# Performance work log

Measured on AMD Instinct MI355X. Metric: run time of the kernel, lower is better.

## Reference

```python
import jax, jax.numpy as jnp
import numpy as np

N = 20000        # genes
E = 100000       # edges per relation
D_IN = 512
HID = 64         # hidden_dim (per-head channels in layers 0,1)
HEADS = 8
D_H = HID * HEADS   # 512 hidden width
D_OUT = 256
NEG_SLOPE = 0.2  # GATv2Conv default negative_slope


def _gatv2(x, src, dst, Wl, bl, Wr, br, att, out_bias, heads, ch):
    """PyG GATv2Conv, add_self_loops=False, concat=True, eval mode (no dropout)."""
    n = x.shape[0]
    xl = (x @ Wl + bl).reshape(n, heads, ch)   # lin_l (source transform)
    xr = (x @ Wr + br).reshape(n, heads, ch)   # lin_r (target transform)
    e = jax.nn.leaky_relu(xl[src] + xr[dst], NEG_SLOPE)   # [E,H,C]
    score = jnp.einsum('ehc,hc->eh', e, att)              # [E,H]
    # segment softmax over incoming edges of each destination node
    m = jax.ops.segment_max(score, dst, num_segments=n)   # [N,H]
    w = jnp.exp(score - m[dst])
    z = jax.ops.segment_sum(w, dst, num_segments=n)
    alpha = w / z[dst]
    out = jax.ops.segment_sum(alpha[:, :, None] * xl[src], dst, num_segments=n)
    return out.reshape(n, heads * ch) + out_bias


def _layernorm(x, g, b):
    mu = x.mean(-1, keepdims=True)
    var = x.var(-1, keepdims=True)
    return (x - mu) * jax.lax.rsqrt(var + 1e-5) * g + b


def setup_inputs() -> dict:
    key = jax.random.key(0)
    ks = jax.random.split(key, 12)
    gn = lambda k, shape, fan_in: (jax.random.normal(k, shape, dtype=jnp.float32)
                                   / np.float32(np.sqrt(fan_in)))
    inp = {}
    inp['x'] = jax.random.normal(ks[0], (N, D_IN), dtype=jnp.float32)
    inp['edge_index'] = jax.random.randint(ks[1], (3, 2, E), 0, N, dtype=jnp.int32)
    # input projection  Linear(512 -> 512)
    inp['proj_w'] = gn(ks[2], (D_IN, D_H), D_IN)
    inp['proj_b'] = jnp.zeros((D_H,), jnp.float32)
    # layers 0,1: stacked over [layer, edge_type]
    inp['l01_lin_l_w'] = gn(ks[3], (2, 3, D_H, D_H), D_H)
    inp['l01_lin_l_b'] = jnp.zeros((2, 3, D_H), jnp.float32)
    inp['l01_lin_r_w'] = gn(ks[4], (2, 3, D_H, D_H), D_H)
    inp['l01_lin_r_b'] = jnp.zeros((2, 3, D_H), jnp.float32)
    inp['l01_att'] = gn(ks[5], (2, 3, HEADS, HID), HID)
    inp['l01_bias'] = jnp.zeros((2, 3, D_H), jnp.float32)
    # layer 2: heads=1, out_channels=256, stacked over edge_type
    inp['l2_lin_l_w'] = gn(ks[6], (3, D_H, D_OUT), D_H)
    inp['l2_lin_l_b'] = jnp.zeros((3, D_OUT), jnp.float32)
    inp['l2_lin_r_w'] = gn(ks[7], (3, D_H, D_OUT), D_H)
    inp['l2_lin_r_b'] = jnp.zeros((3, D_OUT), jnp.float32)
    inp['l2_att'] = gn(ks[8], (3, 1, D_OUT), D_OUT)
    inp['l2_bias'] = jnp.zeros((3, D_OUT), jnp.float32)
    # LayerNorms
    inp['ln01_gamma'] = jnp.ones((2, D_H), jnp.float32)
    inp['ln01_beta'] = jnp.zeros((2, D_H), jnp.float32)
    inp['ln2_gamma'] = jnp.ones((D_OUT,), jnp.float32)
    inp['ln2_beta'] = jnp.zeros((D_OUT,), jnp.float32)
    return inp


def reference(x, edge_index, proj_w, proj_b,
              l01_lin_l_w, l01_lin_l_b, l01_lin_r_w, l01_lin_r_b, l01_att, l01_bias,
              l2_lin_l_w, l2_lin_l_b, l2_lin_r_w, l2_lin_r_b, l2_att, l2_bias,
              ln01_gamma, ln01_beta, ln2_gamma, ln2_beta):
    # input proj + ELU (dropout = identity in eval)
    h = jax.nn.elu(x @ proj_w + proj_b)
    # layers 0 and 1: HeteroConv(sum over 3 relations), ELU, residual, LayerNorm
    for li in range(2):
        res = h
        out = 0.0
        for et in range(3):
            src, dst = edge_index[et, 0], edge_index[et, 1]
            out = out + _gatv2(h, src, dst,
                               l01_lin_l_w[li, et], l01_lin_l_b[li, et],
                               l01_lin_r_w[li, et], l01_lin_r_b[li, et],
                               l01_att[li, et], l01_bias[li, et], HEADS, HID)
        h = jax.nn.elu(out) + res
        h = _layernorm(h, ln01_gamma[li], ln01_beta[li])
    # layer 2: heads=1, out=256; no residual (dims differ)
    out = 0.0
    for et in range(3):
        src, dst = edge_index[et, 0], edge_index[et, 1]
        out = out + _gatv2(h, src, dst,
                           l2_lin_l_w[et], l2_lin_l_b[et],
                           l2_lin_r_w[et], l2_lin_r_b[et],
                           l2_att[et], l2_bias[et], 1, D_OUT)
    h = jax.nn.elu(out)
    return _layernorm(h, ln2_gamma, ln2_beta)
```

## Files before the change

kernel.cpp:

```cpp
#include <hip/hip_runtime.h>


#define NN 20000
#define NE 100000
#define DH 512
#define DOUT 256

typedef __attribute__((ext_vector_type(8))) short short8;
typedef __attribute__((ext_vector_type(4))) short short4v;
typedef __attribute__((ext_vector_type(4))) float f32x4;

__device__ __forceinline__ float b2f(unsigned short s) {
    union { unsigned u; float f; } v; v.u = ((unsigned)s) << 16; return v.f;
}
__device__ __forceinline__ unsigned short f2b(float f) {
    unsigned u = __float_as_uint(f);
    u += 0x7FFFu + ((u >> 16) & 1u);
    return (unsigned short)(u >> 16);
}
__device__ __forceinline__ void load_lds16(const unsigned short* g, unsigned short* l) {
    __builtin_amdgcn_global_load_lds(
        (const __attribute__((address_space(1))) unsigned int*)g,
        (__attribute__((address_space(3))) unsigned int*)l, 16, 0, 0);
}

__global__ void cvt_f2b_k(const float* __restrict__ in,
                          unsigned short* __restrict__ out, int n) {
    int i0 = (blockIdx.x * blockDim.x + threadIdx.x) * 8;
    if (i0 >= n) return;
    #pragma unroll
    for (int j = 0; j < 8; j++) out[i0 + j] = f2b(in[i0 + j]);
}

struct TSeg { const float* in; unsigned short* out; int C; };
struct TTable { TSeg s[19]; };

__global__ void transpose_all_k(TTable t) {
    __shared__ float tile[32][33];
    TSeg d = t.s[blockIdx.y];
    int tiles_x = d.C >> 5;
    int nt = tiles_x << 4;
    if ((int)blockIdx.x >= nt) return;
    int bx = blockIdx.x % tiles_x, by = blockIdx.x / tiles_x;
    int c0 = bx * 32, r0 = by * 32;
    int tx = threadIdx.x & 31, ty = threadIdx.x >> 5;
    #pragma unroll
    for (int i = ty; i < 32; i += 8)
        tile[i][tx] = d.in[(size_t)(r0 + i) * d.C + c0 + tx];
    __syncthreads();
    #pragma unroll
    for (int i = ty; i < 32; i += 8)
        d.out[(size_t)(c0 + i) * 512 + r0 + tx] = f2b(tile[tx][i]);
}

__global__ void count_all_k(const int* __restrict__ ei, int* __restrict__ counts) {
    int i = blockIdx.x * blockDim.x + threadIdx.x;
    if (i >= 3 * NE) return;
    int et = i / NE, idx = i - et * NE;
    int d = ei[(size_t)et * 2 * NE + NE + idx];
    atomicAdd(&counts[et * (NN + 1) + d], 1);
}

__global__ __launch_bounds__(1024)
void scan_par_k(const int* __restrict__ counts, int* __restrict__ offs, int n) {
    __shared__ int part[1024];
    const int* c = counts + (size_t)blockIdx.x * (n + 1);
    int* o = offs + (size_t)blockIdx.x * (n + 1);
    int tid = threadIdx.x;
    int per = (n + 1023) / 1024;
    int base = tid * per;
    int lim = min(base + per, n);
    int sum = 0;
    for (int i = base; i < lim; i++) sum += c[i];
    part[tid] = sum;
    __syncthreads();
    #pragma unroll
    for (int off = 1; off < 1024; off <<= 1) {
        int v = (tid >= off) ? part[tid - off] : 0;
        __syncthreads();
        part[tid] += v;
        __syncthreads();
    }
    int run = part[tid] - sum;
    for (int i = base; i < lim; i++) { o[i] = run; run += c[i]; }
    if (tid == 1023) o[n] = part[1023];
}

__global__ void scatter_all_k(const int* __restrict__ ei, int* __restrict__ cursor,
                              int* __restrict__ srcs_sorted) {
    int i = blockIdx.x * blockDim.x + threadIdx.x;
    if (i >= 3 * NE) return;
    int et = i / NE, idx = i - et * NE;
    int s = ei[(size_t)et * 2 * NE + idx];
    int d = ei[(size_t)et * 2 * NE + NE + idx];
    int p = atomicAdd(&cursor[et * (NN + 1) + d], 1);
    srcs_sorted[(size_t)et * NE + p] = s;
}

template<int ACT, int SEGL2>
__global__ __launch_bounds__(256)
void gemm_k(const unsigned short* __restrict__ A,
            const unsigned short* __restrict__ Bt,
            const float* __restrict__ lb,
            const float* __restrict__ rb,
            unsigned short* __restrict__ Cb,
            int M, int N, int K, int MT, int NT, int STRIPE) {
    __shared__ __align__(16) unsigned short smem[17408];
    unsigned short* As = smem;
    unsigned short* Bs = smem + 8192;
    int bid = blockIdx.x;
    int xcd = bid & 7, r = bid >> 3;
    int mtile = xcd * STRIPE + r / NT;
    int ntile = r % NT;
    if (mtile >= MT) return;
    int bm0 = mtile * 128, bn0 = ntile * 128;

    int tid = threadIdx.x;
    int lane = tid & 63, wave = tid >> 6;
    int quad = lane >> 4, l16 = lane & 15;
    int rw = (wave >> 1) * 64, cw = (wave & 1) * 64;
    int rxor = l16 & 7;

    f32x4 acc[4][4];
    #pragma unroll
    for (int mi = 0; mi < 4; mi++)
        #pragma unroll
        for (int ni = 0; ni < 4; ni++) acc[mi][ni] = (f32x4){0.f, 0.f, 0.f, 0.f};

    for (int k0 = 0; k0 < K; k0 += 64) {
        #pragma unroll
        for (int i = 0; i < 4; i++) {
            int f = i * 256 + tid;
            int row = f >> 3, s = f & 7;
            int cg = s ^ (row & 7);
            load_lds16(A + (size_t)(bm0 + row) * K + k0 + cg * 8, As + f * 8);
        }
        #pragma unroll
        for (int i = 0; i < 4; i++) {
            int f = i * 256 + tid;
            int col = f >> 3, s = f & 7;
            int cg = s ^ (col & 7);
            load_lds16(Bt + (size_t)(bn0 + col) * K + k0 + cg * 8, Bs + f * 8);
        }
        __syncthreads();
        #pragma unroll
        for (int ki = 0; ki < 64; ki += 32) {
            int kch = quad + (ki >> 3);
            int slot = kch ^ rxor;
            short8 af[4], bf[4];
            #pragma unroll
            for (int mi = 0; mi < 4; mi++)
                af[mi] = *(const short8*)(As + (rw + mi * 16 + l16) * 64 + slot * 8);
            #pragma unroll
            for (int ni = 0; ni < 4; ni++)
                bf[ni] = *(const short8*)(Bs + (cw + ni * 16 + l16) * 64 + slot * 8);
            #pragma unroll
            for (int mi = 0; mi < 4; mi++)
                #pragma unroll
                for (int ni = 0; ni < 4; ni++)
                    acc[mi][ni] = __builtin_amdgcn_mfma_f32_16x16x32_bf16(
                        af[mi], bf[ni], acc[mi][ni], 0, 0, 0);
        }
        __syncthreads();
    }

    #pragma unroll
    for (int ni = 0; ni < 4; ni++) {
        int col = cw + ni * 16 + l16;
        int seg = col >> (SEGL2 + 1);
        int lr = (col >> SEGL2) & 1;
        int cc2 = col & ((1 << SEGL2) - 1);
        float bv = (lr ? rb : lb)[(seg << SEGL2) + cc2];
        #pragma unroll
        for (int mi = 0; mi < 4; mi++) {
            int row = rw + mi * 16 + quad * 4;
            #pragma unroll
            for (int i = 0; i < 4; i++) {
                float v = acc[mi][ni][i] + bv;
                if (ACT == 1) v = v > 0.f ? v : expm1f(v);
                smem[(row + i) * 136 + col] = f2b(v);
            }
        }
    }
    __syncthreads();
    #pragma unroll
    for (int it = 0; it < 8; it++) {
        int chunk = it * 256 + tid;
        int row = chunk >> 4, cc = chunk & 15;
        int grow = bm0 + row;
        if (grow < M) {
            uint4 d = *(const uint4*)(smem + row * 136 + cc * 8);
            *(uint4*)(Cb + (size_t)grow * N + bn0 + cc * 8) = d;
        }
    }
}

__global__ __launch_bounds__(192)
void gat_fused01_k(const unsigned short* __restrict__ C,
                   const int* __restrict__ offs3,
                   const int* __restrict__ srcs3,
                   const float* __restrict__ att,
                   const float* __restrict__ bias3,
                   unsigned short* __restrict__ hb,
                   const float* __restrict__ gamma,
                   const float* __restrict__ beta,
                   int n_nodes) {
    const unsigned LD = 3072;
    __shared__ float lds_tot[2 * DH];
    int tid = threadIdx.x;
    int lane = tid & 63, et = tid >> 6;
    int n = blockIdx.x;
    int c0 = lane * 8;

    const int* offs = offs3 + et * (NN + 1);
    const int* srcs = srcs3 + (size_t)et * NE;
    int e0 = offs[n], e1 = offs[n + 1];

    float tot[8];
    #pragma unroll
    for (int j = 0; j < 8; j++) tot[j] = 0.f;

    if (e0 < e1) {
        const unsigned short* XL = C + et * 1024 + c0;
        float xr[8], at[8];
        {
            short8 t = *(const short8*)(C + (size_t)n * LD + et * 1024 + 512 + c0);
            #pragma unroll
            for (int j = 0; j < 8; j++) xr[j] = b2f((unsigned short)t[j]);
            #pragma unroll
            for (int j = 0; j < 8; j++) at[j] = att[et * 512 + c0 + j];
        }
        float z = 0.f, acc[8];
        #pragma unroll
        for (int j = 0; j < 8; j++) acc[j] = 0.f;

        auto G = [&](int idx) {
            return *(const short8*)(XL + (unsigned)srcs[idx] * LD);
        };
        auto process = [&](short8 cur) {
            float xl[8];
            #pragma unroll
            for (int j = 0; j < 8; j++) xl[j] = b2f((unsigned short)cur[j]);
            float p = 0.f;
            #pragma unroll
            for (int j = 0; j < 8; j++) {
                float v = xl[j] + xr[j];
                v = fmaxf(v, 0.2f * v);
                p = fmaf(v, at[j], p);
            }
            p += __shfl_xor(p, 1, 64);
            p += __shfl_xor(p, 2, 64);
            p += __shfl_xor(p, 4, 64);
            float wgt = __expf(p);
            z += wgt;
            #pragma unroll
            for (int j = 0; j < 8; j++) acc[j] = fmaf(wgt, xl[j], acc[j]);
        };

        int ef = e0, eb = e1 - 1;
        short8 a0 = G(ef);
        short8 a1 = G(min(ef + 1, eb));
        short8 b0 = G(eb);
        short8 b1 = G(max(eb - 1, ef));
        while (ef < eb) {
            short8 ca = a0; a0 = a1; a1 = G(min(ef + 2, eb));
            short8 cb = b0; b0 = b1; b1 = G(max(eb - 2, ef));
            process(ca);
            process(cb);
            ef++; eb--;
        }
        if (ef == eb) process(a0);

        float inv = 1.f / z;
        #pragma unroll
        for (int j = 0; j < 8; j++) tot[j] = acc[j] * inv;
    }

    if (et) {
        float* dst = lds_tot + (et - 1) * DH + lane;
        #pragma unroll
        for (int j = 0; j < 8; j++) dst[j * 64] = tot[j];
    }
    __syncthreads();
    if (et == 0) {
        unsigned short* hrow = hb + (size_t)n * DH + c0;
        short8 rt = *(const short8*)hrow;
        float v[8]; float s1 = 0.f;
        #pragma unroll
        for (int j = 0; j < 8; j++) {
            int c = c0 + j;
            float x = tot[j] + lds_tot[j * 64 + lane] + lds_tot[DH + j * 64 + lane]
                    + bias3[c] + bias3[512 + c] + bias3[1024 + c];
            x = x > 0.f ? x : expm1f(x);
            x += b2f((unsigned short)rt[j]);
            v[j] = x; s1 += x;
        }
        #pragma unroll
        for (int off = 1; off < 64; off <<= 1) s1 += __shfl_xor(s1, off, 64);
        float mean = s1 * (1.f / DH);
        float s2 = 0.f;
        #pragma unroll
        for (int j = 0; j < 8; j++) { float d = v[j] - mean; s2 += d * d; }
        #pragma unroll
        for (int off = 1; off < 64; off <<= 1) s2 += __shfl_xor(s2, off, 64);
        float rstd = rsqrtf(s2 * (1.f / DH) + 1e-5f);
        short8 ov;
        #pragma unroll
        for (int j = 0; j < 8; j++) {
            int c = c0 + j;
            ov[j] = (short)f2b((v[j] - mean) * rstd * gamma[c] + beta[c]);
        }
        *(short8*)hrow = ov;
    }
    (void)n_nodes;
}

__global__ __launch_bounds__(192)
void gat_fused2_k(const unsigned short* __restrict__ C,
                  const int* __restrict__ offs3,
                  const int* __restrict__ srcs3,
                  const float* __restrict__ att,
                  const float* __restrict__ bias3,
                  const float* __restrict__ gamma,
                  const float* __restrict__ beta,
                  float* __restrict__ out, int n_nodes) {
    const unsigned LD = 1536;
    __shared__ float lds_tot[2 * DOUT];
    int tid = threadIdx.x;
    int lane = tid & 63, et = tid >> 6;
    int n = blockIdx.x;
    int c0 = lane * 4;

    const int* offs = offs3 + et * (NN + 1);
    const int* srcs = srcs3 + (size_t)et * NE;
    int e0 = offs[n], e1 = offs[n + 1];

    float tot[4] = {0.f, 0.f, 0.f, 0.f};

    if (e0 < e1) {
        const unsigned short* XL = C + et * 512 + c0;
        float xr[4], at[4];
        {
            short4v t = *(const short4v*)(C + (size_t)n * LD + et * 512 + 256 + c0);
            #pragma unroll
            for (int j = 0; j < 4; j++) xr[j] = b2f((unsigned short)t[j]);
            #pragma unroll
            for (int j = 0; j < 4; j++) at[j] = att[et * 256 + c0 + j];
        }
        float z = 0.f, acc[4] = {0.f, 0.f, 0.f, 0.f};

        auto G = [&](int idx) {
            return *(const short4v*)(XL + (unsigned)srcs[idx] * LD);
        };
        auto process = [&](short4v cur) {
            float xl[4];
            #pragma unroll
            for (int j = 0; j < 4; j++) xl[j] = b2f((unsigned short)cur[j]);
            float p = 0.f;
            #pragma unroll
            for (int j = 0; j < 4; j++) {
                float v = xl[j] + xr[j];
                v = fmaxf(v, 0.2f * v);
                p = fmaf(v, at[j], p);
            }
            #pragma unroll
            for (int off = 1; off < 64; off <<= 1) p += __shfl_xor(p, off, 64);
            float wgt = __expf(p);
            z += wgt;
            #pragma unroll
            for (int j = 0; j < 4; j++) acc[j] = fmaf(wgt, xl[j], acc[j]);
        };

        int ef = e0, eb = e1 - 1;
        short4v a0 = G(ef);
        short4v a1 = G(min(ef + 1, eb));
        short4v b0 = G(eb);
        short4v b1 = G(max(eb - 1, ef));
        while (ef < eb) {
            short4v ca = a0; a0 = a1; a1 = G(min(ef + 2, eb));
            short4v cb = b0; b0 = b1; b1 = G(max(eb - 2, ef));
            process(ca);
            process(cb);
            ef++; eb--;
        }
        if (ef == eb) process(a0);

        float inv = 1.f / z;
        #pragma unroll
        for (int j = 0; j < 4; j++) tot[j] = acc[j] * inv;
    }

    if (et) {
        float* dst = lds_tot + (et - 1) * DOUT + lane;
        #pragma unroll
        for (int j = 0; j < 4; j++) dst[j * 64] = tot[j];
    }
    __syncthreads();
    if (et == 0) {
        float v[4]; float s1 = 0.f;
        #pragma unroll
        for (int j = 0; j < 4; j++) {
            int c = c0 + j;
            float x = tot[j] + lds_tot[j * 64 + lane] + lds_tot[DOUT + j * 64 + lane]
                    + bias3[c] + bias3[256 + c] + bias3[512 + c];
            x = x > 0.f ? x : expm1f(x);
            v[j] = x; s1 += x;
        }
        #pragma unroll
        for (int off = 1; off < 64; off <<= 1) s1 += __shfl_xor(s1, off, 64);
        float mean = s1 * (1.f / DOUT);
        float s2 = 0.f;
        #pragma unroll
        for (int j = 0; j < 4; j++) { float d = v[j] - mean; s2 += d * d; }
        #pragma unroll
        for (int off = 1; off < 64; off <<= 1) s2 += __shfl_xor(s2, off, 64);
        float rstd = rsqrtf(s2 * (1.f / DOUT) + 1e-5f);
        f32x4 o;
        #pragma unroll
        for (int j = 0; j < 4; j++) {
            int c = c0 + j;
            o[j] = (v[j] - mean) * rstd * gamma[c] + beta[c];
        }
        *(f32x4*)(out + (size_t)n * DOUT + c0) = o;
    }
    (void)n_nodes;
}

extern "C" void kernel_launch(void* const* d_in, const int* in_sizes, int n_in,
                              void* d_out, int out_size, void* d_ws, size_t ws_size,
                              hipStream_t stream) {
    const float* x       = (const float*)d_in[0];
    const int*   ei      = (const int*)d_in[1];
    const float* proj_w  = (const float*)d_in[2];
    const float* proj_b  = (const float*)d_in[3];
    const float* l01lw   = (const float*)d_in[4];
    const float* l01lb   = (const float*)d_in[5];
    const float* l01rw   = (const float*)d_in[6];
    const float* l01rb   = (const float*)d_in[7];
    const float* l01att  = (const float*)d_in[8];
    const float* l01bias = (const float*)d_in[9];
    const float* l2lw    = (const float*)d_in[10];
    const float* l2lb    = (const float*)d_in[11];
    const float* l2rw    = (const float*)d_in[12];
    const float* l2rb    = (const float*)d_in[13];
    const float* l2att   = (const float*)d_in[14];
    const float* l2bias  = (const float*)d_in[15];
    const float* g01     = (const float*)d_in[16];
    const float* b01     = (const float*)d_in[17];
    const float* g2      = (const float*)d_in[18];
    const float* b2      = (const float*)d_in[19];
    (void)in_sizes; (void)n_in; (void)out_size; (void)ws_size;

    char* w = (char*)d_ws;
    size_t off = 0;
    auto carve = [&](size_t bytes) { void* p = w + off; off = (off + bytes + 255) & ~(size_t)255; return p; };
    unsigned short* h_b     = (unsigned short*)carve((size_t)NN * DH * 2);
    unsigned short* xb      = (unsigned short*)carve((size_t)NN * DH * 2);
    unsigned short* Cbuf    = (unsigned short*)carve((size_t)NN * 3072 * 2);
    unsigned short* Wt      = (unsigned short*)carve((size_t)4194304 * 2);
    int*            counts3 = (int*)           carve((size_t)3 * (NN + 1) * 4);
    int*            offs3   = (int*)           carve((size_t)3 * (NN + 1) * 4);
    int*            srcs3   = (int*)           carve((size_t)3 * NE * 4);
    carve(65536);

    unsigned short* Wt_proj = Wt;
    unsigned short* Wt_L0   = Wt_proj + 262144;
    unsigned short* Wt_L1   = Wt_L0 + 3072 * 512;
    unsigned short* Wt_L2   = Wt_L1 + 3072 * 512;

    dim3 tb(256);
    const int MT = (NN + 127) / 128;
    const int STRIPE = (MT + 7) / 8;

    cvt_f2b_k<<<dim3(5000), tb, 0, stream>>>(x, xb, NN * DH);
    TTable tt;
    {
        int s = 0;
        tt.s[s++] = {proj_w, Wt_proj, 512};
        for (int li = 0; li < 2; li++) {
            unsigned short* base = li ? Wt_L1 : Wt_L0;
            for (int et = 0; et < 3; et++)
                tt.s[s++] = {l01lw + (size_t)(li * 3 + et) * 262144,
                             base + (size_t)et * 2 * 262144, 512};
            for (int et = 0; et < 3; et++)
                tt.s[s++] = {l01rw + (size_t)(li * 3 + et) * 262144,
                             base + 262144 + (size_t)et * 2 * 262144, 512};
        }
        for (int et = 0; et < 3; et++)
            tt.s[s++] = {l2lw + (size_t)et * 131072,
                         Wt_L2 + (size_t)et * 2 * 131072, 256};
        for (int et = 0; et < 3; et++)
            tt.s[s++] = {l2rw + (size_t)et * 131072,
                         Wt_L2 + 131072 + (size_t)et * 2 * 131072, 256};
    }
    transpose_all_k<<<dim3(256, 19), tb, 0, stream>>>(tt);

    hipMemsetAsync(counts3, 0, (size_t)3 * (NN + 1) * 4, stream);
    count_all_k<<<dim3((3 * NE + 255) / 256), tb, 0, stream>>>(ei, counts3);
    scan_par_k<<<dim3(3), dim3(1024), 0, stream>>>(counts3, offs3, NN);
    hipMemcpyAsync(counts3, offs3, (size_t)3 * (NN + 1) * 4,
                   hipMemcpyDeviceToDevice, stream);
    scatter_all_k<<<dim3((3 * NE + 255) / 256), tb, 0, stream>>>(ei, counts3, srcs3);

    gemm_k<1, 9><<<dim3(8 * STRIPE * 4), tb, 0, stream>>>(
        xb, Wt_proj, proj_b, proj_b, h_b, NN, 512, 512, MT, 4, STRIPE);

    for (int li = 0; li < 2; li++) {
        gemm_k<0, 9><<<dim3(8 * STRIPE * 24), tb, 0, stream>>>(
            h_b, li ? Wt_L1 : Wt_L0,
            l01lb + (size_t)li * 3 * 512, l01rb + (size_t)li * 3 * 512,
            Cbuf, NN, 3072, 512, MT, 24, STRIPE);
        gat_fused01_k<<<dim3(NN), dim3(192), 0, stream>>>(
            Cbuf, offs3, srcs3,
            l01att + (size_t)li * 3 * 512, l01bias + (size_t)li * 3 * 512,
            h_b, g01 + (size_t)li * DH, b01 + (size_t)li * DH, NN);
    }

    gemm_k<0, 8><<<dim3(8 * STRIPE * 12), tb, 0, stream>>>(
        h_b, Wt_L2, l2lb, l2rb, Cbuf, NN, 1536, 512, MT, 12, STRIPE);
    gat_fused2_k<<<dim3(NN), dim3(192), 0, stream>>>(
        Cbuf, offs3, srcs3, l2att, l2bias, g2, b2, (float*)d_out, NN);
}
```

Measured before the change: 642.5 us.

## Replace 128x128 GEMM with 256x256 double-buffered LDS-prefetch GEMM kernel

Swaps the 128x128, 256-thread bf16 MFMA GEMM for a 256x256, 512-thread kernel. It double-buffers A/B tiles in LDS and issues the next k-tile's global-to-LDS loads between the MFMA phases, raising wave priority around the MFMA blocks. Larger tiles raise operand reuse per LDS load and the prefetch is meant to hide global latency. The cost is a 128KB LDS footprint (one block per CU), more grid quantization/tail effects over 79 row tiles, and a two-pass epilogue to stage the output through LDS.

```diff
diff --git a/kernel.cpp b/kernel.cpp
--- a/kernel.cpp
+++ b/kernel.cpp
@@ -98,99 +98,138 @@
 }
 
 template<int ACT, int SEGL2>
-__global__ __launch_bounds__(256)
-void gemm_k(const unsigned short* __restrict__ A,
-            const unsigned short* __restrict__ Bt,
-            const float* __restrict__ lb,
-            const float* __restrict__ rb,
-            unsigned short* __restrict__ Cb,
-            int M, int N, int K, int MT, int NT, int STRIPE) {
-    __shared__ __align__(16) unsigned short smem[17408];
-    unsigned short* As = smem;
-    unsigned short* Bs = smem + 8192;
+__global__ __launch_bounds__(512, 2)
+void gemm256_k(const unsigned short* __restrict__ A,
+               const unsigned short* __restrict__ Bt,
+               const float* __restrict__ lb,
+               const float* __restrict__ rb,
+               unsigned short* __restrict__ Cb,
+               int M, int N, int K, int MT, int NT) {
+    __shared__ __align__(16) unsigned short smem[65536];
+
     int bid = blockIdx.x;
-    int xcd = bid & 7, r = bid >> 3;
-    int mtile = xcd * STRIPE + r / NT;
-    int ntile = r % NT;
-    if (mtile >= MT) return;
-    int bm0 = mtile * 128, bn0 = ntile * 128;
+    int nwg = MT * NT;
+    int q = nwg >> 3, r = nwg & 7;
+    int xcd = bid & 7;
+    int wg = (xcd < r ? xcd * (q + 1) : r * (q + 1) + (xcd - r) * q) + (bid >> 3);
+    int mtile = wg / NT, ntile = wg % NT;
+    int bm0 = mtile * 256, bn0 = ntile * 256;
 
     int tid = threadIdx.x;
-    int lane = tid & 63, wave = tid >> 6;
+    int lane = tid & 63, wid = tid >> 6;
+    int wr = wid >> 2, wc = wid & 3;
     int quad = lane >> 4, l16 = lane & 15;
-    int rw = (wave >> 1) * 64, cw = (wave & 1) * 64;
+    int rbase = wr * 128, cbase = wc * 64;
     int rxor = l16 & 7;
 
-    f32x4 acc[4][4];
-    #pragma unroll
-    for (int mi = 0; mi < 4; mi++)
-        #pragma unroll
-        for (int ni = 0; ni < 4; ni++) acc[mi][ni] = (f32x4){0.f, 0.f, 0.f, 0.f};
-
-    for (int k0 = 0; k0 < K; k0 += 64) {
-        #pragma unroll
-        for (int i = 0; i < 4; i++) {
-            int f = i * 256 + tid;
-            int row = f >> 3, s = f & 7;
-            int cg = s ^ (row & 7);
-            load_lds16(A + (size_t)(bm0 + row) * K + k0 + cg * 8, As + f * 8);
-        }
-        #pragma unroll
-        for (int i = 0; i < 4; i++) {
-            int f = i * 256 + tid;
-            int col = f >> 3, s = f & 7;
-            int cg = s ^ (col & 7);
-            load_lds16(Bt + (size_t)(bn0 + col) * K + k0 + cg * 8, Bs + f * 8);
-        }
+    f32x4 acc[8][4];
+    #pragma unroll
+    for (int m = 0; m < 8; m++)
+        #pragma unroll
+        for (int n = 0; n < 4; n++) acc[m][n] = (f32x4){0.f, 0.f, 0.f, 0.f};
+
+    const int NKT = K >> 6;
+
+    #pragma unroll
+    for (int ld = 0; ld < 4; ld++) {
+        int f = ld * 512 + tid;
+        int row = f >> 3, s = f & 7;
+        int cg = s ^ (row & 7);
+        load_lds16(A + (size_t)(bm0 + row) * K + cg * 8, smem + f * 8);
+        load_lds16(Bt + (size_t)(bn0 + row) * K + cg * 8, smem + 16384 + f * 8);
+    }
+    asm volatile("s_waitcnt vmcnt(0)" ::: "memory");
+    __syncthreads();
+
+    for (int kt = 0; kt < NKT; kt++) {
+        const unsigned short* Asr = smem + (kt & 1) * 32768;
+        const unsigned short* Bsr = Asr + 16384;
+        unsigned short* Asw = smem + ((kt + 1) & 1) * 32768;
+        unsigned short* Bsw = Asw + 16384;
+        bool st = (kt + 1 < NKT);
+        int kk = (kt + 1) << 6;
+        short8 bfr[4][2];
+
+        #pragma unroll
+        for (int p = 0; p < 4; p++) {
+            if (p == 0) {
+                #pragma unroll
+                for (int n = 0; n < 4; n++)
+                    #pragma unroll
+                    for (int s2 = 0; s2 < 2; s2++)
+                        bfr[n][s2] = *(const short8*)(Bsr +
+                            (cbase + n * 16 + l16) * 64 +
+                            ((quad + s2 * 4) ^ rxor) * 8);
+            }
+            short8 af[2][2];
+            #pragma unroll
+            for (int mi = 0; mi < 2; mi++)
+                #pragma unroll
+                for (int s2 = 0; s2 < 2; s2++)
+                    af[mi][s2] = *(const short8*)(Asr +
+                        (rbase + (2 * p + mi) * 16 + l16) * 64 +
+                        ((quad + s2 * 4) ^ rxor) * 8);
+
+            if (st) {
+                int f = p * 512 + tid;
+                int row = f >> 3, s = f & 7;
+                int cg = s ^ (row & 7);
+                load_lds16(A + (size_t)(bm0 + row) * K + kk + cg * 8, Asw + f * 8);
+                load_lds16(Bt + (size_t)(bn0 + row) * K + kk + cg * 8, Bsw + f * 8);
+            }
+
+            __builtin_amdgcn_s_barrier();
+            asm volatile("s_waitcnt lgkmcnt(0)" ::: "memory");
+            __builtin_amdgcn_sched_barrier(0);
+            __builtin_amdgcn_s_setprio(1);
+            #pragma unroll
+            for (int mi = 0; mi < 2; mi++)
+                #pragma unroll
+                for (int n = 0; n < 4; n++)
+                    #pragma unroll
+                    for (int s2 = 0; s2 < 2; s2++)
+                        acc[2 * p + mi][n] = __builtin_amdgcn_mfma_f32_16x16x32_bf16(
+                            af[mi][s2], bfr[n][s2], acc[2 * p + mi][n], 0, 0, 0);
+            __builtin_amdgcn_s_setprio(0);
+            if (p == 3) asm volatile("s_waitcnt vmcnt(0)" ::: "memory");
+            __builtin_amdgcn_s_barrier();
+        }
+    }
+
+    #pragma unroll
+    for (int h = 0; h < 2; h++) {
         __syncthreads();
-        #pragma unroll
-        for (int ki = 0; ki < 64; ki += 32) {
-            int kch = quad + (ki >> 3);
-            int slot = kch ^ rxor;
-            short8 af[4], bf[4];
-            #pragma unroll
-            for (int mi = 0; mi < 4; mi++)
-                af[mi] = *(const short8*)(As + (rw + mi * 16 + l16) * 64 + slot * 8);
-            #pragma unroll
-            for (int ni = 0; ni < 4; ni++)
-                bf[ni] = *(const short8*)(Bs + (cw + ni * 16 + l16) * 64 + slot * 8);
-            #pragma unroll
-            for (int mi = 0; mi < 4; mi++)
+        if (wr == h) {
+            #pragma unroll
+            for (int n = 0; n < 4; n++) {
+                int col = cbase + n * 16 + l16;
+                int gcol = bn0 + col;
+                int seg = gcol >> (SEGL2 + 1);
+                int lr = (gcol >> SEGL2) & 1;
+                int cc2 = gcol & ((1 << SEGL2) - 1);
+                float bv = (lr ? rb : lb)[(seg << SEGL2) + cc2];
                 #pragma unroll
-                for (int ni = 0; ni < 4; ni++)
-                    acc[mi][ni] = __builtin_amdgcn_mfma_f32_16x16x32_bf16(
-                        af[mi], bf[ni], acc[mi][ni], 0, 0, 0);
+                for (int m = 0; m < 8; m++) {
+                    int lrow = m * 16 + quad * 4;
+                    #pragma unroll
+                    for (int i = 0; i < 4; i++) {
+                        float v = acc[m][n][i] + bv;
+                        if (ACT == 1) v = v > 0.f ? v : expm1f(v);
+                        smem[(lrow + i) * 264 + col] = f2b(v);
+                    }
+                }
+            }
         }
         __syncthreads();
-    }
-
-    #pragma unroll
-    for (int ni = 0; ni < 4; ni++) {
-        int col = cw + ni * 16 + l16;
-        int seg = col >> (SEGL2 + 1);
-        int lr = (col >> SEGL2) & 1;
-        int cc2 = col & ((1 << SEGL2) - 1);
-        float bv = (lr ? rb : lb)[(seg << SEGL2) + cc2];
-        #pragma unroll
-        for (int mi = 0; mi < 4; mi++) {
-            int row = rw + mi * 16 + quad * 4;
-            #pragma unroll
-            for (int i = 0; i < 4; i++) {
-                float v = acc[mi][ni][i] + bv;
-                if (ACT == 1) v = v > 0.f ? v : expm1f(v);
-                smem[(row + i) * 136 + col] = f2b(v);
+        #pragma unroll
+        for (int it = 0; it < 8; it++) {
+            int chunk = it * 512 + tid;
+            int row = chunk >> 5, cc = chunk & 31;
+            int grow = bm0 + h * 128 + row;
+            if (grow < M) {
+                uint4 d = *(const uint4*)(smem + row * 264 + cc * 8);
+                *(uint4*)(Cb + (size_t)grow * N + bn0 + cc * 8) = d;
             }
-        }
-    }
-    __syncthreads();
-    #pragma unroll
-    for (int it = 0; it < 8; it++) {
-        int chunk = it * 256 + tid;
-        int row = chunk >> 4, cc = chunk & 15;
-        int grow = bm0 + row;
-        if (grow < M) {
-            uint4 d = *(const uint4*)(smem + row * 136 + cc * 8);
-            *(uint4*)(Cb + (size_t)grow * N + bn0 + cc * 8) = d;
         }
     }
 }
@@ -469,8 +508,7 @@
     unsigned short* Wt_L2   = Wt_L1 + 3072 * 512;
 
     dim3 tb(256);
-    const int MT = (NN + 127) / 128;
-    const int STRIPE = (MT + 7) / 8;
+    const int MT = (NN + 255) / 256;
 
     cvt_f2b_k<<<dim3(5000), tb, 0, stream>>>(x, xb, NN * DH);
     TTable tt;
@@ -502,22 +540,22 @@
                    hipMemcpyDeviceToDevice, stream);
     scatter_all_k<<<dim3((3 * NE + 255) / 256), tb, 0, stream>>>(ei, counts3, srcs3);
 
-    gemm_k<1, 9><<<dim3(8 * STRIPE * 4), tb, 0, stream>>>(
-        xb, Wt_proj, proj_b, proj_b, h_b, NN, 512, 512, MT, 4, STRIPE);
+    gemm256_k<1, 9><<<dim3(MT * 2), dim3(512), 0, stream>>>(
+        xb, Wt_proj, proj_b, proj_b, h_b, NN, 512, 512, MT, 2);
 
     for (int li = 0; li < 2; li++) {
-        gemm_k<0, 9><<<dim3(8 * STRIPE * 24), tb, 0, stream>>>(
+        gemm256_k<0, 9><<<dim3(MT * 12), dim3(512), 0, stream>>>(
             h_b, li ? Wt_L1 : Wt_L0,
             l01lb + (size_t)li * 3 * 512, l01rb + (size_t)li * 3 * 512,
-            Cbuf, NN, 3072, 512, MT, 24, STRIPE);
+            Cbuf, NN, 3072, 512, MT, 12);
         gat_fused01_k<<<dim3(NN), dim3(192), 0, stream>>>(
             Cbuf, offs3, srcs3,
             l01att + (size_t)li * 3 * 512, l01bias + (size_t)li * 3 * 512,
             h_b, g01 + (size_t)li * DH, b01 + (size_t)li * DH, NN);
     }
 
-    gemm_k<0, 8><<<dim3(8 * STRIPE * 12), tb, 0, stream>>>(
-        h_b, Wt_L2, l2lb, l2rb, Cbuf, NN, 1536, 512, MT, 12, STRIPE);
+    gemm256_k<0, 8><<<dim3(MT * 6), dim3(512), 0, stream>>>(
+        h_b, Wt_L2, l2lb, l2rb, Cbuf, NN, 1536, 512, MT, 6);
     gat_fused2_k<<<dim3(NN), dim3(192), 0, stream>>>(
         Cbuf, offs3, srcs3, l2att, l2bias, g2, b2, (float*)d_out, NN);
 }
```

Result: slower. 670.6 us (+4.4%).
